# Kernel tuning notes

Measured on AMD Instinct MI355X. Metric: run time of the kernel, lower is better.

## Reference

```python
import jax, jax.numpy as jnp
import numpy as np

N_HEADS = 16
EMBED_DIM = 1024
HEAD_DIM = EMBED_DIM // N_HEADS
SEQ_LEN = 2048


def setup_inputs() -> dict:
    key = jax.random.key(0)
    ks = jax.random.split(key, 9)
    s = 1.0 / np.sqrt(EMBED_DIM)
    inp = {
        "x": jax.random.normal(ks[0], (SEQ_LEN, EMBED_DIM), dtype=jnp.float32),
        "Wq": jax.random.uniform(ks[1], (EMBED_DIM, EMBED_DIM), jnp.float32, -s, s),
        "bq": jax.random.uniform(ks[2], (EMBED_DIM,), jnp.float32, -s, s),
        "Wk": jax.random.uniform(ks[3], (EMBED_DIM, EMBED_DIM), jnp.float32, -s, s),
        "bk": jax.random.uniform(ks[4], (EMBED_DIM,), jnp.float32, -s, s),
        "Wv": jax.random.uniform(ks[5], (EMBED_DIM, EMBED_DIM), jnp.float32, -s, s),
        "bv": jax.random.uniform(ks[6], (EMBED_DIM,), jnp.float32, -s, s),
        "Wo": jax.random.uniform(ks[7], (EMBED_DIM, EMBED_DIM), jnp.float32, -s, s),
        "bo": jax.random.uniform(ks[8], (EMBED_DIM,), jnp.float32, -s, s),
    }
    return inp


def reference(x, Wq, bq, Wk, bk, Wv, bv, Wo, bo):
    # Linear layers (torch convention: y = x @ W.T + b)
    Q = x @ Wq.T + bq  # [S, E]
    K = x @ Wk.T + bk
    V = x @ Wv.T + bv
    # split heads -> [H, S, D]
    def split(t):
        return t.reshape(SEQ_LEN, N_HEADS, HEAD_DIM).transpose(1, 0, 2)
    Qh, Kh, Vh = split(Q), split(K), split(V)
    # NOTE: faithful to source, scale is sqrt(embed_dim), not sqrt(head_dim)
    scale = 1.0 / np.sqrt(EMBED_DIM)
    scores = jnp.einsum("hsd,htd->hst", Qh, Kh) * scale  # [H, S, S]
    attn = jax.nn.softmax(scores, axis=-1)
    ctx = jnp.einsum("hst,htd->hsd", attn, Vh)  # [H, S, D]
    ctx = ctx.transpose(1, 0, 2).reshape(SEQ_LEN, EMBED_DIM)
    out = ctx @ Wo.T + bo
    return (out, attn)
```

## Files before the change

kernel.cpp:

```cpp
#include <hip/hip_runtime.h>
#include <hip/hip_bf16.h>
#include <stdint.h>

#define SQL 2048
#define EMB 1024
#define NHD 16
#define HDD 64

typedef __bf16 bf16x8 __attribute__((ext_vector_type(8)));
typedef __bf16 bf16x4 __attribute__((ext_vector_type(4)));
typedef float f32x4 __attribute__((ext_vector_type(4)));

__device__ __forceinline__ f32x4 mfma16(bf16x8 a, bf16x8 b, f32x4 c) {
    return __builtin_amdgcn_mfma_f32_16x16x32_bf16(a, b, c, 0, 0, 0);
}

__device__ __forceinline__ void gload_lds16(const __bf16* g, __bf16* lds) {
    __builtin_amdgcn_global_load_lds(
        (const __attribute__((address_space(1))) uint32_t*)g,
        (__attribute__((address_space(3))) uint32_t*)lds,
        16, 0, 0);
}

__global__ void cast5_kernel(const float* __restrict__ x, const float* __restrict__ wq,
                             const float* __restrict__ wk, const float* __restrict__ wv,
                             const float* __restrict__ wo, __bf16* __restrict__ out)
{
    int i = blockIdx.x * blockDim.x + threadIdx.x;
    const float* src; int off;
    if      (i < (512 << 10))  { src = x;  off = 0; }
    else if (i < (768 << 10))  { src = wq; off = 512 << 10; }
    else if (i < (1024 << 10)) { src = wk; off = 768 << 10; }
    else if (i < (1280 << 10)) { src = wv; off = 1024 << 10; }
    else                       { src = wo; off = 1280 << 10; }
    float4 v = ((const float4*)src)[i - off];
    bf16x4 o;
    o[0] = (__bf16)v.x; o[1] = (__bf16)v.y; o[2] = (__bf16)v.z; o[3] = (__bf16)v.w;
    ((bf16x4*)out)[i] = o;
}

template<bool OUT_BF16>
__global__ __launch_bounds__(256, 2)
void gemm_bt(const __bf16* __restrict__ A,
             const __bf16* __restrict__ B0, const __bf16* __restrict__ B1, const __bf16* __restrict__ B2,
             const float* __restrict__ bias0, const float* __restrict__ bias1, const float* __restrict__ bias2,
             void* __restrict__ out0, void* __restrict__ out1, void* __restrict__ out2,
             float s0, float s1, float s2,
             int M, int N, int K)
{
    const __bf16* B = B0; const float* bias = bias0; void* Cout = out0; float cscale = s0;
    if (blockIdx.z == 1) { B = B1; bias = bias1; Cout = out1; cscale = s1; }
    if (blockIdx.z == 2) { B = B2; bias = bias2; Cout = out2; cscale = s2; }

    __shared__ __attribute__((aligned(16))) __bf16 As[128 * 32];
    __shared__ __attribute__((aligned(16))) __bf16 Bs[128 * 32];

    const int tid  = threadIdx.x;
    const int lane = tid & 63;
    const int wave = tid >> 6;
    const int lrow = lane & 15;
    const int quad = lane >> 4;
    const int bm = blockIdx.y * 128;
    const int bn = blockIdx.x * 128;
    const int wm = (wave >> 1) * 64;
    const int wn = (wave & 1) * 64;

    const f32x4 fzero = {0.f, 0.f, 0.f, 0.f};
    f32x4 acc[4][4];
#pragma unroll
    for (int i = 0; i < 4; i++)
#pragma unroll
        for (int j = 0; j < 4; j++) acc[i][j] = fzero;

    const int srow = (lane >> 2);
    const int scol = (lane & 3) * 8;

    for (int k0 = 0; k0 < K; k0 += 32) {
        __syncthreads();
#pragma unroll
        for (int i = 0; i < 2; i++) {
            int rbase = wave * 32 + i * 16;
            gload_lds16(&A[(size_t)(bm + rbase + srow) * K + k0 + scol], &As[rbase * 32]);
            gload_lds16(&B[(size_t)(bn + rbase + srow) * K + k0 + scol], &Bs[rbase * 32]);
        }
        __syncthreads();
        bf16x8 af[4], bfr[4];
#pragma unroll
        for (int i = 0; i < 4; i++) af[i]  = *(const bf16x8*)&As[(wm + i * 16 + lrow) * 32 + quad * 8];
#pragma unroll
        for (int i = 0; i < 4; i++) bfr[i] = *(const bf16x8*)&Bs[(wn + i * 16 + lrow) * 32 + quad * 8];
#pragma unroll
        for (int mi = 0; mi < 4; mi++)
#pragma unroll
            for (int ni = 0; ni < 4; ni++)
                acc[mi][ni] = mfma16(af[mi], bfr[ni], acc[mi][ni]);
    }

#pragma unroll
    for (int mi = 0; mi < 4; mi++) {
        int row = bm + wm + mi * 16 + quad * 4;
#pragma unroll
        for (int ni = 0; ni < 4; ni++) {
            int col = bn + wn + ni * 16 + lrow;
            float bv = bias[col];
#pragma unroll
            for (int r = 0; r < 4; r++) {
                float v = (acc[mi][ni][r] + bv) * cscale;
                if (OUT_BF16) ((__bf16*)Cout)[(size_t)(row + r) * N + col] = (__bf16)v;
                else          ((float*)Cout)[(size_t)(row + r) * N + col] = v;
            }
        }
    }
}

__global__ __launch_bounds__(256, 2)
void transpose_v(const __bf16* __restrict__ V, __bf16* __restrict__ Vt) {
    __shared__ __attribute__((aligned(16))) __bf16 tile[64][72];
    const int tid = threadIdx.x;
    const int s0 = blockIdx.x * 64;
    const int c0 = blockIdx.y * 64;
#pragma unroll
    for (int i = 0; i < 2; i++) {
        int lin = tid + i * 256;
        int r  = lin >> 3;
        int cg = (lin & 7) << 3;
        *(bf16x8*)&tile[r][cg] = *(const bf16x8*)&V[(size_t)(s0 + r) * EMB + c0 + cg];
    }
    __syncthreads();
#pragma unroll
    for (int i = 0; i < 2; i++) {
        int lin = tid + i * 256;
        int c  = lin >> 3;
        int sg = (lin & 7) << 3;
        bf16x8 t;
#pragma unroll
        for (int j = 0; j < 8; j++) t[j] = tile[sg + j][c];
        *(bf16x8*)&Vt[(size_t)(c0 + c) * SQL + s0 + sg] = t;
    }
}

__global__ __launch_bounds__(256, 2)
void attn_kernel(const __bf16* __restrict__ Qg, const __bf16* __restrict__ Kg,
                 const __bf16* __restrict__ Vt, float* __restrict__ attn,
                 __bf16* __restrict__ ctx)
{
    __shared__ __attribute__((aligned(16))) __bf16 Ps[4][32][40];
    __shared__ float MLb[2][2][2][16][2];
    __shared__ float Ored[64][66];

    const int tid  = threadIdx.x;
    const int lane = tid & 63;
    const int w    = tid >> 6;
    const int wq   = w & 1;
    const int wk   = w >> 1;
    const int lrow = lane & 15;
    const int quad = lane >> 4;
    const int h  = blockIdx.y;
    const int q0 = blockIdx.x * 64;
    const f32x4 fzero = {0.f, 0.f, 0.f, 0.f};

    bf16x8 qf[2][2];
#pragma unroll
    for (int qg = 0; qg < 2; qg++) {
        const size_t qoff = (size_t)(q0 + wq * 32 + qg * 16 + lrow) * EMB + h * HDD;
        qf[qg][0] = *(const bf16x8*)&Qg[qoff + quad * 8];
        qf[qg][1] = *(const bf16x8*)&Qg[qoff + 32 + quad * 8];
    }

    float m[2] = {-1e30f, -1e30f}, l[2] = {0.f, 0.f};

    for (int k0 = 0; k0 < SQL; k0 += 64) {
        f32x4 st[2][2];
#pragma unroll
        for (int kt = 0; kt < 2; kt++) {
            const __bf16* kp = &Kg[(size_t)(k0 + wk * 32 + kt * 16 + lrow) * EMB + h * HDD];
            bf16x8 b0 = *(const bf16x8*)&kp[quad * 8];
            bf16x8 b1 = *(const bf16x8*)&kp[32 + quad * 8];
#pragma unroll
            for (int qg = 0; qg < 2; qg++) {
                f32x4 a = mfma16(b0, qf[qg][0], fzero);
                st[qg][kt] = mfma16(b1, qf[qg][1], a);
            }
        }
#pragma unroll
        for (int qg = 0; qg < 2; qg++) {
            float tm = -1e30f;
#pragma unroll
            for (int kt = 0; kt < 2; kt++)
#pragma unroll
                for (int r = 0; r < 4; r++) tm = fmaxf(tm, st[qg][kt][r]);
            tm = fmaxf(tm, __shfl_xor(tm, 16));
            tm = fmaxf(tm, __shfl_xor(tm, 32));
            float mn = fmaxf(m[qg], tm);
            float rs = 0.f;
#pragma unroll
            for (int kt = 0; kt < 2; kt++)
#pragma unroll
                for (int r = 0; r < 4; r++) rs += __expf(st[qg][kt][r] - mn);
            rs += __shfl_xor(rs, 16);
            rs += __shfl_xor(rs, 32);
            l[qg] = l[qg] * __expf(m[qg] - mn) + rs;
            m[qg] = mn;
        }
    }

    if (quad == 0) {
#pragma unroll
        for (int qg = 0; qg < 2; qg++) {
            MLb[wk][wq][qg][lrow][0] = m[qg];
            MLb[wk][wq][qg][lrow][1] = l[qg];
        }
    }
    __syncthreads();
    float rinv[2];
#pragma unroll
    for (int qg = 0; qg < 2; qg++) {
        float mo = MLb[wk ^ 1][wq][qg][lrow][0];
        float lo = MLb[wk ^ 1][wq][qg][lrow][1];
        float mf = fmaxf(m[qg], mo);
        float lf = l[qg] * __expf(m[qg] - mf) + lo * __expf(mo - mf);
        m[qg] = mf;
        rinv[qg] = 1.f / lf;
    }

    f32x4 o[2][4];
#pragma unroll
    for (int qg = 0; qg < 2; qg++)
#pragma unroll
        for (int nt = 0; nt < 4; nt++) o[qg][nt] = fzero;

    float* arow[2];
#pragma unroll
    for (int qg = 0; qg < 2; qg++)
        arow[qg] = attn + (size_t)h * SQL * SQL + (size_t)(q0 + wq * 32 + qg * 16 + lrow) * SQL;

    for (int k0 = 0; k0 < SQL; k0 += 64) {
        bf16x8 vf[4];
#pragma unroll
        for (int nt = 0; nt < 4; nt++)
            vf[nt] = *(const bf16x8*)&Vt[(size_t)(h * HDD + nt * 16 + lrow) * SQL + k0 + wk * 32 + quad * 8];

#pragma unroll
        for (int kt = 0; kt < 2; kt++) {
            const __bf16* kp = &Kg[(size_t)(k0 + wk * 32 + kt * 16 + lrow) * EMB + h * HDD];
            bf16x8 b0 = *(const bf16x8*)&kp[quad * 8];
            bf16x8 b1 = *(const bf16x8*)&kp[32 + quad * 8];
#pragma unroll
            for (int qg = 0; qg < 2; qg++) {
                f32x4 a = mfma16(b0, qf[qg][0], fzero);
                a = mfma16(b1, qf[qg][1], a);
                f32x4 pv; bf16x4 pb;
#pragma unroll
                for (int r = 0; r < 4; r++) {
                    float p = __expf(a[r] - m[qg]) * rinv[qg];
                    pv[r] = p; pb[r] = (__bf16)p;
                }
                *(f32x4*)&arow[qg][k0 + wk * 32 + kt * 16 + quad * 4] = pv;
                *(bf16x4*)&Ps[w][qg * 16 + lrow][kt * 16 + quad * 4] = pb;
            }
        }
        bf16x8 pf[2];
#pragma unroll
        for (int qg = 0; qg < 2; qg++)
            pf[qg] = *(const bf16x8*)&Ps[w][qg * 16 + lrow][quad * 8];
#pragma unroll
        for (int nt = 0; nt < 4; nt++)
#pragma unroll
            for (int qg = 0; qg < 2; qg++)
                o[qg][nt] = mfma16(pf[qg], vf[nt], o[qg][nt]);
    }

    if (wk == 1) {
#pragma unroll
        for (int qg = 0; qg < 2; qg++)
#pragma unroll
            for (int nt = 0; nt < 4; nt++)
#pragma unroll
                for (int r = 0; r < 4; r++)
                    Ored[wq * 32 + qg * 16 + quad * 4 + r][nt * 16 + lrow] = o[qg][nt][r];
    }
    __syncthreads();
    if (wk == 0) {
#pragma unroll
        for (int qg = 0; qg < 2; qg++)
#pragma unroll
            for (int nt = 0; nt < 4; nt++)
#pragma unroll
                for (int r = 0; r < 4; r++) {
                    int qrow = wq * 32 + qg * 16 + quad * 4 + r;
                    float v = o[qg][nt][r] + Ored[qrow][nt * 16 + lrow];
                    ctx[(size_t)(q0 + qrow) * EMB + h * HDD + nt * 16 + lrow] = (__bf16)v;
                }
    }
}

extern "C" void kernel_launch(void* const* d_in, const int* in_sizes, int n_in,
                              void* d_out, int out_size, void* d_ws, size_t ws_size,
                              hipStream_t stream)
{
    const float* x  = (const float*)d_in[0];
    const float* Wq = (const float*)d_in[1];
    const float* bq = (const float*)d_in[2];
    const float* Wk = (const float*)d_in[3];
    const float* bk = (const float*)d_in[4];
    const float* Wv = (const float*)d_in[5];
    const float* bv = (const float*)d_in[6];
    const float* Wo = (const float*)d_in[7];
    const float* bo = (const float*)d_in[8];

    float* out  = (float*)d_out;
    float* attn = out + (size_t)SQL * EMB;

    const size_t M1 = 1u << 20;
    __bf16* wsb = (__bf16*)d_ws;
    __bf16* xb  = wsb;
    __bf16* wqb = wsb + 2 * M1;
    __bf16* wkb = wsb + 3 * M1;
    __bf16* wvb = wsb + 4 * M1;
    __bf16* wob = wsb + 5 * M1;
    __bf16* Qb  = wsb + 6 * M1;
    __bf16* Kb  = wsb + 8 * M1;
    __bf16* Vb  = wsb + 10 * M1;
    __bf16* Vtb = wsb + 12 * M1;
    __bf16* ctb = wsb + 14 * M1;

    cast5_kernel<<<6144, 256, 0, stream>>>(x, Wq, Wk, Wv, Wo, wsb);

    gemm_bt<true><<<dim3(EMB / 128, SQL / 128, 3), 256, 0, stream>>>(
        xb, wqb, wkb, wvb, bq, bk, bv,
        (void*)Qb, (void*)Kb, (void*)Vb,
        0.03125f, 1.0f, 1.0f, SQL, EMB, EMB);

    transpose_v<<<dim3(SQL / 64, EMB / 64), 256, 0, stream>>>(Vb, Vtb);

    attn_kernel<<<dim3(SQL / 64, NHD), 256, 0, stream>>>(Qb, Kb, Vtb, attn, ctb);

    gemm_bt<false><<<dim3(EMB / 128, SQL / 128, 1), 256, 0, stream>>>(
        ctb, wob, wob, wob, bo, bo, bo,
        (void*)out, (void*)out, (void*)out,
        1.0f, 1.0f, 1.0f, SQL, EMB, EMB);
}
```

Baseline: 424.8 us.

## Stage K/V tiles in swizzled LDS with double buffering and 32x32 MFMA

The attention kernel now cooperatively loads K and V^T tiles into double-buffered, XOR-swizzled LDS with global_load_lds, prefetching the next tile while the current one is computed. Before, each wave read its fragments straight from global memory. Both passes switch from 16x16x32 to 32x32x16 bf16 MFMA, which changes the fragment layout and the final ctx reduction and store pattern. This cuts redundant global loads and uses fewer, larger MFMAs, at the cost of a block-wide barrier every iteration and more LDS per block, which may limit occupancy.

```diff
diff --git a/kernel.cpp b/kernel.cpp
--- a/kernel.cpp
+++ b/kernel.cpp
@@ -10,9 +10,13 @@
 typedef __bf16 bf16x8 __attribute__((ext_vector_type(8)));
 typedef __bf16 bf16x4 __attribute__((ext_vector_type(4)));
 typedef float f32x4 __attribute__((ext_vector_type(4)));
+typedef float f32x16 __attribute__((ext_vector_type(16)));
 
 __device__ __forceinline__ f32x4 mfma16(bf16x8 a, bf16x8 b, f32x4 c) {
     return __builtin_amdgcn_mfma_f32_16x16x32_bf16(a, b, c, 0, 0, 0);
+}
+__device__ __forceinline__ f32x16 mfma32(bf16x8 a, bf16x8 b, f32x16 c) {
+    return __builtin_amdgcn_mfma_f32_32x32x16_bf16(a, b, c, 0, 0, 0);
 }
 
 __device__ __forceinline__ void gload_lds16(const __bf16* g, __bf16* lds) {
@@ -144,8 +148,10 @@
                  const __bf16* __restrict__ Vt, float* __restrict__ attn,
                  __bf16* __restrict__ ctx)
 {
-    __shared__ __attribute__((aligned(16))) __bf16 Ps[4][32][40];
-    __shared__ float MLb[2][2][2][16][2];
+    __shared__ __attribute__((aligned(16))) __bf16 Ks[2][64 * 64];
+    __shared__ __attribute__((aligned(16))) __bf16 Vs[2][64 * 64];
+    __shared__ __attribute__((aligned(16))) __bf16 Ps[4][32 * 40];
+    __shared__ float MLb[2][2][32][2];
     __shared__ float Ored[64][66];
 
     const int tid  = threadIdx.x;
@@ -153,144 +159,149 @@
     const int w    = tid >> 6;
     const int wq   = w & 1;
     const int wk   = w >> 1;
-    const int lrow = lane & 15;
-    const int quad = lane >> 4;
+    const int l31  = lane & 31;
+    const int hi   = lane >> 5;
     const int h  = blockIdx.y;
     const int q0 = blockIdx.x * 64;
-    const f32x4 fzero = {0.f, 0.f, 0.f, 0.f};
-
-    bf16x8 qf[2][2];
-#pragma unroll
-    for (int qg = 0; qg < 2; qg++) {
-        const size_t qoff = (size_t)(q0 + wq * 32 + qg * 16 + lrow) * EMB + h * HDD;
-        qf[qg][0] = *(const bf16x8*)&Qg[qoff + quad * 8];
-        qf[qg][1] = *(const bf16x8*)&Qg[qoff + 32 + quad * 8];
-    }
-
-    float m[2] = {-1e30f, -1e30f}, l[2] = {0.f, 0.f};
-
-    for (int k0 = 0; k0 < SQL; k0 += 64) {
-        f32x4 st[2][2];
+
+    const int srow  = lane >> 3;
+    const int sslot = (lane & 7) ^ (srow & 7);
+
+    auto stageK = [&](int buf, int k0) {
+#pragma unroll
+        for (int j = 0; j < 2; j++) {
+            int r = w * 16 + j * 8;
+            gload_lds16(&Kg[(size_t)(k0 + r + srow) * EMB + h * HDD + sslot * 8],
+                        &Ks[buf][r * 64]);
+        }
+    };
+    auto stageV = [&](int buf, int k0) {
+#pragma unroll
+        for (int j = 0; j < 2; j++) {
+            int r = w * 16 + j * 8;
+            gload_lds16(&Vt[(size_t)(h * HDD + r + srow) * SQL + k0 + sslot * 8],
+                        &Vs[buf][r * 64]);
+        }
+    };
+
+    bf16x8 qf[4];
+    {
+        const __bf16* qp = &Qg[(size_t)(q0 + wq * 32 + l31) * EMB + h * HDD + hi * 8];
+#pragma unroll
+        for (int ds = 0; ds < 4; ds++) qf[ds] = *(const bf16x8*)&qp[ds * 16];
+    }
+
+    const f32x16 Z16 = {0.f,0.f,0.f,0.f,0.f,0.f,0.f,0.f,0.f,0.f,0.f,0.f,0.f,0.f,0.f,0.f};
+    const int krowoff = (wk * 32 + l31) * 64;
+    const int lane7   = lane & 7;
+
+    float sm_m = -1e30f, sm_l = 0.f;
+    int buf = 0;
+
+    stageK(0, 0);
+    __syncthreads();
+    for (int t = 0; t < 32; t++) {
+        if (t < 31) stageK(buf ^ 1, (t + 1) * 64);
+        f32x16 s = Z16;
+#pragma unroll
+        for (int ds = 0; ds < 4; ds++) {
+            bf16x8 kf = *(const bf16x8*)&Ks[buf][krowoff + ((((ds << 1) | hi) ^ lane7) << 3)];
+            s = mfma32(kf, qf[ds], s);
+        }
+        float tm = s[0];
+#pragma unroll
+        for (int r = 1; r < 16; r++) tm = fmaxf(tm, s[r]);
+        tm = fmaxf(tm, __shfl_xor(tm, 32));
+        float mn = fmaxf(sm_m, tm);
+        float rs = 0.f;
+#pragma unroll
+        for (int r = 0; r < 16; r++) rs += __expf(s[r] - mn);
+        rs += __shfl_xor(rs, 32);
+        sm_l = sm_l * __expf(sm_m - mn) + rs;
+        sm_m = mn;
+        __syncthreads();
+        buf ^= 1;
+    }
+
+    if (lane < 32) { MLb[wk][wq][lane][0] = sm_m; MLb[wk][wq][lane][1] = sm_l; }
+    stageK(0, 0);
+    stageV(0, 0);
+    __syncthreads();
+    float rinv;
+    {
+        float mo = MLb[wk ^ 1][wq][l31][0];
+        float lo = MLb[wk ^ 1][wq][l31][1];
+        float mf = fmaxf(sm_m, mo);
+        float lf = sm_l * __expf(sm_m - mf) + lo * __expf(mo - mf);
+        sm_m = mf;
+        rinv = 1.f / lf;
+    }
+
+    f32x16 o0 = Z16, o1 = Z16;
+    float* __restrict__ arow = attn + (size_t)h * SQL * SQL + (size_t)(q0 + wq * 32 + l31) * SQL;
+    const int vrow0 = l31 * 64;
+    const int vrow1 = (32 + l31) * 64;
+    const int psrow = l31 * 40;
+
+    buf = 0;
+    for (int t = 0; t < 32; t++) {
+        const int k0 = t * 64;
+        if (t < 31) { stageK(buf ^ 1, k0 + 64); stageV(buf ^ 1, k0 + 64); }
+        f32x16 s = Z16;
+#pragma unroll
+        for (int ds = 0; ds < 4; ds++) {
+            bf16x8 kf = *(const bf16x8*)&Ks[buf][krowoff + ((((ds << 1) | hi) ^ lane7) << 3)];
+            s = mfma32(kf, qf[ds], s);
+        }
+#pragma unroll
+        for (int g = 0; g < 4; g++) {
+            f32x4 pv; bf16x4 pb;
+#pragma unroll
+            for (int i = 0; i < 4; i++) {
+                float p = __expf(s[g * 4 + i] - sm_m) * rinv;
+                pv[i] = p; pb[i] = (__bf16)p;
+            }
+            *(f32x4*)&arow[k0 + wk * 32 + g * 8 + hi * 4] = pv;
+            *(bf16x4*)&Ps[w][psrow + g * 8 + hi * 4] = pb;
+        }
 #pragma unroll
         for (int kt = 0; kt < 2; kt++) {
-            const __bf16* kp = &Kg[(size_t)(k0 + wk * 32 + kt * 16 + lrow) * EMB + h * HDD];
-            bf16x8 b0 = *(const bf16x8*)&kp[quad * 8];
-            bf16x8 b1 = *(const bf16x8*)&kp[32 + quad * 8];
-#pragma unroll
-            for (int qg = 0; qg < 2; qg++) {
-                f32x4 a = mfma16(b0, qf[qg][0], fzero);
-                st[qg][kt] = mfma16(b1, qf[qg][1], a);
+            bf16x8 pf = *(const bf16x8*)&Ps[w][psrow + kt * 16 + hi * 8];
+            int vslot = (((wk << 2) | (kt << 1) | hi) ^ lane7) << 3;
+            bf16x8 v0 = *(const bf16x8*)&Vs[buf][vrow0 + vslot];
+            bf16x8 v1 = *(const bf16x8*)&Vs[buf][vrow1 + vslot];
+            o0 = mfma32(v0, pf, o0);
+            o1 = mfma32(v1, pf, o1);
+        }
+        __syncthreads();
+        buf ^= 1;
+    }
+
+    if (wk == 1) {
+#pragma unroll
+        for (int g = 0; g < 4; g++)
+#pragma unroll
+            for (int i = 0; i < 4; i++) {
+                int dl = i + g * 8 + hi * 4;
+                Ored[dl][wq * 32 + l31]      = o0[g * 4 + i];
+                Ored[32 + dl][wq * 32 + l31] = o1[g * 4 + i];
             }
-        }
-#pragma unroll
-        for (int qg = 0; qg < 2; qg++) {
-            float tm = -1e30f;
-#pragma unroll
-            for (int kt = 0; kt < 2; kt++)
-#pragma unroll
-                for (int r = 0; r < 4; r++) tm = fmaxf(tm, st[qg][kt][r]);
-            tm = fmaxf(tm, __shfl_xor(tm, 16));
-            tm = fmaxf(tm, __shfl_xor(tm, 32));
-            float mn = fmaxf(m[qg], tm);
-            float rs = 0.f;
-#pragma unroll
-            for (int kt = 0; kt < 2; kt++)
-#pragma unroll
-                for (int r = 0; r < 4; r++) rs += __expf(st[qg][kt][r] - mn);
-            rs += __shfl_xor(rs, 16);
-            rs += __shfl_xor(rs, 32);
-            l[qg] = l[qg] * __expf(m[qg] - mn) + rs;
-            m[qg] = mn;
-        }
-    }
-
-    if (quad == 0) {
-#pragma unroll
-        for (int qg = 0; qg < 2; qg++) {
-            MLb[wk][wq][qg][lrow][0] = m[qg];
-            MLb[wk][wq][qg][lrow][1] = l[qg];
-        }
-    }
-    __syncthreads();
-    float rinv[2];
-#pragma unroll
-    for (int qg = 0; qg < 2; qg++) {
-        float mo = MLb[wk ^ 1][wq][qg][lrow][0];
-        float lo = MLb[wk ^ 1][wq][qg][lrow][1];
-        float mf = fmaxf(m[qg], mo);
-        float lf = l[qg] * __expf(m[qg] - mf) + lo * __expf(mo - mf);
-        m[qg] = mf;
-        rinv[qg] = 1.f / lf;
-    }
-
-    f32x4 o[2][4];
-#pragma unroll
-    for (int qg = 0; qg < 2; qg++)
-#pragma unroll
-        for (int nt = 0; nt < 4; nt++) o[qg][nt] = fzero;
-
-    float* arow[2];
-#pragma unroll
-    for (int qg = 0; qg < 2; qg++)
-        arow[qg] = attn + (size_t)h * SQL * SQL + (size_t)(q0 + wq * 32 + qg * 16 + lrow) * SQL;
-
-    for (int k0 = 0; k0 < SQL; k0 += 64) {
-        bf16x8 vf[4];
-#pragma unroll
-        for (int nt = 0; nt < 4; nt++)
-            vf[nt] = *(const bf16x8*)&Vt[(size_t)(h * HDD + nt * 16 + lrow) * SQL + k0 + wk * 32 + quad * 8];
-
-#pragma unroll
-        for (int kt = 0; kt < 2; kt++) {
-            const __bf16* kp = &Kg[(size_t)(k0 + wk * 32 + kt * 16 + lrow) * EMB + h * HDD];
-            bf16x8 b0 = *(const bf16x8*)&kp[quad * 8];
-            bf16x8 b1 = *(const bf16x8*)&kp[32 + quad * 8];
-#pragma unroll
-            for (int qg = 0; qg < 2; qg++) {
-                f32x4 a = mfma16(b0, qf[qg][0], fzero);
-                a = mfma16(b1, qf[qg][1], a);
-                f32x4 pv; bf16x4 pb;
-#pragma unroll
-                for (int r = 0; r < 4; r++) {
-                    float p = __expf(a[r] - m[qg]) * rinv[qg];
-                    pv[r] = p; pb[r] = (__bf16)p;
-                }
-                *(f32x4*)&arow[qg][k0 + wk * 32 + kt * 16 + quad * 4] = pv;
-                *(bf16x4*)&Ps[w][qg * 16 + lrow][kt * 16 + quad * 4] = pb;
-            }
-        }
-        bf16x8 pf[2];
-#pragma unroll
-        for (int qg = 0; qg < 2; qg++)
-            pf[qg] = *(const bf16x8*)&Ps[w][qg * 16 + lrow][quad * 8];
-#pragma unroll
-        for (int nt = 0; nt < 4; nt++)
-#pragma unroll
-            for (int qg = 0; qg < 2; qg++)
-                o[qg][nt] = mfma16(pf[qg], vf[nt], o[qg][nt]);
-    }
-
-    if (wk == 1) {
-#pragma unroll
-        for (int qg = 0; qg < 2; qg++)
-#pragma unroll
-            for (int nt = 0; nt < 4; nt++)
-#pragma unroll
-                for (int r = 0; r < 4; r++)
-                    Ored[wq * 32 + qg * 16 + quad * 4 + r][nt * 16 + lrow] = o[qg][nt][r];
     }
     __syncthreads();
     if (wk == 0) {
-#pragma unroll
-        for (int qg = 0; qg < 2; qg++)
-#pragma unroll
-            for (int nt = 0; nt < 4; nt++)
-#pragma unroll
-                for (int r = 0; r < 4; r++) {
-                    int qrow = wq * 32 + qg * 16 + quad * 4 + r;
-                    float v = o[qg][nt][r] + Ored[qrow][nt * 16 + lrow];
-                    ctx[(size_t)(q0 + qrow) * EMB + h * HDD + nt * 16 + lrow] = (__bf16)v;
-                }
+        __bf16* crow = &ctx[(size_t)(q0 + wq * 32 + l31) * EMB + h * HDD];
+#pragma unroll
+        for (int g = 0; g < 4; g++) {
+            bf16x4 c0, c1;
+#pragma unroll
+            for (int i = 0; i < 4; i++) {
+                int dl = i + g * 8 + hi * 4;
+                c0[i] = (__bf16)(o0[g * 4 + i] + Ored[dl][wq * 32 + l31]);
+                c1[i] = (__bf16)(o1[g * 4 + i] + Ored[32 + dl][wq * 32 + l31]);
+            }
+            *(bf16x4*)&crow[g * 8 + hi * 4]      = c0;
+            *(bf16x4*)&crow[32 + g * 8 + hi * 4] = c1;
+        }
     }
 }
 
```

Result: faster. 413.9 us (-2.6%).
